# Kernel tuning notes

Measured on AMD Instinct MI355X. Metric: run time of the kernel, lower is better.

Reference implementation:

```python
import jax, jax.numpy as jnp
import numpy as np

POOL_OUT = 100  # AdaptiveAvgPool1d target length
SCALE = np.sqrt(256.0).astype(np.float32)


def setup_inputs() -> dict:
    key = jax.random.key(0)
    ks = jax.random.split(key, 5)
    B, F, T = 16, 512, 4000
    x = jax.random.normal(ks[0], (B, F, T), dtype=jnp.float32)
    Wk = jax.random.normal(ks[1], (256, 100), dtype=jnp.float32) * 0.05
    bk = jax.random.normal(ks[2], (256,), dtype=jnp.float32) * 0.05
    Wq = jax.random.normal(ks[3], (256, 100), dtype=jnp.float32) * 0.05
    bq = jax.random.normal(ks[4], (256,), dtype=jnp.float32) * 0.05
    return {"x": x, "Wk": Wk, "bk": bk, "Wq": Wq, "bq": bq}


def reference(x, Wk, bk, Wq, bq):
    B, F, T = x.shape
    # AdaptiveAvgPool1d(100): T divisible by 100 -> mean over contiguous windows
    pooled = x.reshape(B, F, POOL_OUT, T // POOL_OUT).mean(axis=-1)  # [B,F,100]
    key = pooled @ Wk.T + bk    # [B,F,256]
    query = pooled @ Wq.T + bq  # [B,F,256]
    att = jax.nn.softmax(jnp.einsum('bfd,bgd->bfg', key, query) / SCALE, axis=2)  # [B,F,F]
    # the per-step loop sum+concat is exactly att @ x
    cat = jnp.einsum('bfg,bgt->bft', att, x)  # [B,F,T]
    fw = cat.mean(axis=2, keepdims=True)      # [B,F,1]
    mi = fw.min(axis=1, keepdims=True)
    ma = fw.max(axis=1, keepdims=True)
    fw_n = (fw - mi) / (ma - mi) + 1e-6
    return x * fw_n
```

## Files before the change

### kernel.cpp

```cpp
#include <hip/hip_runtime.h>
#include <math.h>

#define B_ 16
#define F_ 512
#define T_ 4000
#define D_ 100
#define E_ 256
#define ROWS (B_*F_)

__global__ __launch_bounds__(256) void k_pool(const float* __restrict__ x,
                                              float* __restrict__ pooled,
                                              float* __restrict__ xmean) {
    __shared__ float part[4];
    const int row = blockIdx.x;
    const int tid = threadIdx.x;
    float s = 0.f;
    if (tid < 200) {
        const float4* p = (const float4*)(x + (size_t)row * T_ + 20 * tid);
        float4 a0 = p[0], a1 = p[1], a2 = p[2], a3 = p[3], a4 = p[4];
        s  = a0.x + a0.y + a0.z + a0.w;
        s += a1.x + a1.y + a1.z + a1.w;
        s += a2.x + a2.y + a2.z + a2.w;
        s += a3.x + a3.y + a3.z + a3.w;
        s += a4.x + a4.y + a4.z + a4.w;
    }
    float other = __shfl_xor(s, 1);
    if (tid < 200 && (tid & 1) == 0)
        pooled[(size_t)row * D_ + (tid >> 1)] = (s + other) * (1.0f/40.0f);
    float tot = s;
    #pragma unroll
    for (int off = 32; off; off >>= 1) tot += __shfl_xor(tot, off);
    if ((tid & 63) == 0) part[tid >> 6] = tot;
    __syncthreads();
    if (tid == 0)
        xmean[row] = (part[0] + part[1] + part[2] + part[3]) * (1.0f/(float)T_);
}

__global__ __launch_bounds__(256) void k_kq(const float* __restrict__ pooled,
                                            const float* __restrict__ Wk,
                                            const float* __restrict__ bk,
                                            const float* __restrict__ Wq,
                                            const float* __restrict__ bq,
                                            float* __restrict__ KQ) {
    __shared__ float As[D_][65];
    __shared__ float Bs[D_][65];
    const int m0 = blockIdx.x * 64;
    const int n0 = blockIdx.y * 64;
    const int tid = threadIdx.x;

    const float* Ab = pooled + (size_t)m0 * D_;
    for (int i = tid; i < 64 * D_; i += 256) {
        int r = i / D_, k = i - r * D_;
        As[k][r] = Ab[i];
    }
    const float* Wb = (n0 < E_) ? (Wk + (size_t)n0 * D_) : (Wq + (size_t)(n0 - E_) * D_);
    for (int i = tid; i < 64 * D_; i += 256) {
        int r = i / D_, k = i - r * D_;
        Bs[k][r] = Wb[i];
    }
    __syncthreads();

    const int tm = (tid >> 4) * 4;
    const int tn = (tid & 15) * 4;
    float acc[4][4] = {};
    for (int k = 0; k < D_; ++k) {
        float a[4], b[4];
        #pragma unroll
        for (int i = 0; i < 4; ++i) a[i] = As[k][tm + i];
        #pragma unroll
        for (int j = 0; j < 4; ++j) b[j] = Bs[k][tn + j];
        #pragma unroll
        for (int i = 0; i < 4; ++i)
            #pragma unroll
            for (int j = 0; j < 4; ++j)
                acc[i][j] = fmaf(a[i], b[j], acc[i][j]);
    }
    #pragma unroll
    for (int i = 0; i < 4; ++i)
        #pragma unroll
        for (int j = 0; j < 4; ++j) {
            int n = n0 + tn + j;
            float bias = (n < E_) ? bk[n] : bq[n - E_];
            KQ[(size_t)(m0 + tm + i) * 512 + n] = acc[i][j] + bias;
        }
}

__global__ __launch_bounds__(256) void k_scores(const float* __restrict__ KQ,
                                                float* __restrict__ S) {
    __shared__ float As[64][68];
    __shared__ float Bs[64][68];
    const int b  = blockIdx.z;
    const int f0 = blockIdx.x * 64;
    const int g0 = blockIdx.y * 64;
    const float* Ab = KQ + ((size_t)b * F_ + f0) * 512;
    const float* Bb = KQ + ((size_t)b * F_ + g0) * 512 + E_;
    const int tid = threadIdx.x;
    const int tm = (tid >> 4) * 4;
    const int tn = (tid & 15) * 4;
    float acc[4][4] = {};
    for (int ks = 0; ks < E_; ks += 64) {
        for (int i = tid; i < 64 * 64; i += 256) {
            int r = i >> 6, kk = i & 63;
            As[kk][r] = Ab[(size_t)r * 512 + ks + kk];
            Bs[kk][r] = Bb[(size_t)r * 512 + ks + kk];
        }
        __syncthreads();
        #pragma unroll 16
        for (int k = 0; k < 64; ++k) {
            float4 a4 = *(const float4*)(&As[k][tm]);
            float4 b4 = *(const float4*)(&Bs[k][tn]);
            float a[4] = {a4.x, a4.y, a4.z, a4.w};
            float b[4] = {b4.x, b4.y, b4.z, b4.w};
            #pragma unroll
            for (int i = 0; i < 4; ++i)
                #pragma unroll
                for (int j = 0; j < 4; ++j)
                    acc[i][j] = fmaf(a[i], b[j], acc[i][j]);
        }
        __syncthreads();
    }
    float* Sb = S + ((size_t)b * F_ + f0) * 512 + g0;
    #pragma unroll
    for (int i = 0; i < 4; ++i)
        #pragma unroll
        for (int j = 0; j < 4; ++j)
            Sb[(size_t)(tm + i) * 512 + tn + j] = acc[i][j] * (1.0f/16.0f);
}

__global__ __launch_bounds__(256) void k_softmax_fw(const float* __restrict__ S,
                                                    const float* __restrict__ xmean,
                                                    float* __restrict__ fw) {
    const int row  = blockIdx.x * 4 + (threadIdx.x >> 6);
    const int lane = threadIdx.x & 63;
    const int b    = row >> 9;
    const float4* Sr = (const float4*)(S + (size_t)row * 512);
    const float4* xm = (const float4*)(xmean + ((size_t)b << 9));
    float4 v0 = Sr[lane * 2], v1 = Sr[lane * 2 + 1];
    float m = fmaxf(fmaxf(fmaxf(v0.x, v0.y), fmaxf(v0.z, v0.w)),
                    fmaxf(fmaxf(v1.x, v1.y), fmaxf(v1.z, v1.w)));
    #pragma unroll
    for (int off = 32; off; off >>= 1) m = fmaxf(m, __shfl_xor(m, off));
    float4 x0 = xm[lane * 2], x1 = xm[lane * 2 + 1];
    float sum = 0.f, dot = 0.f, p;
    p = expf(v0.x - m); sum += p; dot += p * x0.x;
    p = expf(v0.y - m); sum += p; dot += p * x0.y;
    p = expf(v0.z - m); sum += p; dot += p * x0.z;
    p = expf(v0.w - m); sum += p; dot += p * x0.w;
    p = expf(v1.x - m); sum += p; dot += p * x1.x;
    p = expf(v1.y - m); sum += p; dot += p * x1.y;
    p = expf(v1.z - m); sum += p; dot += p * x1.z;
    p = expf(v1.w - m); sum += p; dot += p * x1.w;
    #pragma unroll
    for (int off = 32; off; off >>= 1) {
        sum += __shfl_xor(sum, off);
        dot += __shfl_xor(dot, off);
    }
    if (lane == 0) fw[row] = dot / sum;
}

__global__ __launch_bounds__(512) void k_norm(const float* __restrict__ fw,
                                              float* __restrict__ fwn) {
    __shared__ float rmin[512];
    __shared__ float rmax[512];
    const int b = blockIdx.x, tid = threadIdx.x;
    float v = fw[b * F_ + tid];
    rmin[tid] = v; rmax[tid] = v;
    __syncthreads();
    for (int s = 256; s > 0; s >>= 1) {
        if (tid < s) {
            rmin[tid] = fminf(rmin[tid], rmin[tid + s]);
            rmax[tid] = fmaxf(rmax[tid], rmax[tid + s]);
        }
        __syncthreads();
    }
    float mi = rmin[0], ma = rmax[0];
    fwn[b * F_ + tid] = (v - mi) / (ma - mi) + 1e-6f;
}

__global__ __launch_bounds__(256) void k_scale(const float* __restrict__ x,
                                               const float* __restrict__ fwn,
                                               float* __restrict__ out) {
    const int row = blockIdx.x;
    const float s = fwn[row];
    const float4* xr = (const float4*)(x + (size_t)row * T_);
    float4* orow = (float4*)(out + (size_t)row * T_);
    for (int i = threadIdx.x; i < T_/4; i += 256) {
        float4 v = xr[i];
        v.x *= s; v.y *= s; v.z *= s; v.w *= s;
        orow[i] = v;
    }
}

extern "C" void kernel_launch(void* const* d_in, const int* in_sizes, int n_in,
                              void* d_out, int out_size, void* d_ws, size_t ws_size,
                              hipStream_t stream) {
    const float* x  = (const float*)d_in[0];
    const float* Wk = (const float*)d_in[1];
    const float* bk = (const float*)d_in[2];
    const float* Wq = (const float*)d_in[3];
    const float* bq = (const float*)d_in[4];
    float* out = (float*)d_out;

    float* ws     = (float*)d_ws;
    float* pooled = ws;
    float* xmean  = pooled + (size_t)ROWS * D_;
    float* KQ     = xmean + ROWS;
    float* S      = KQ + (size_t)ROWS * 512;
    float* fw     = S + (size_t)B_ * F_ * F_;
    float* fwn    = fw + ROWS;

    k_pool<<<ROWS, 256, 0, stream>>>(x, pooled, xmean);
    k_kq<<<dim3(ROWS/64, 512/64), 256, 0, stream>>>(pooled, Wk, bk, Wq, bq, KQ);
    k_scores<<<dim3(F_/64, F_/64, B_), 256, 0, stream>>>(KQ, S);
    k_softmax_fw<<<ROWS/4, 256, 0, stream>>>(S, xmean, fw);
    k_norm<<<B_, 512, 0, stream>>>(fw, fwn);
    k_scale<<<ROWS, 256, 0, stream>>>(x, fwn, out);
}
```

Measured before the change: 321.1 us.

## Use split-bf16 MFMA for attention scores with pre-tiled K/Q layout

The projection kernel now writes K and Q as hi/lo bf16 pairs in a fragment-ready tiled layout. The score kernel uses bf16 MFMA 16x16x32 with three products (hh, hl, lh) to approximate fp32 accuracy, replacing the FP32 FMA tiled GEMM and its shared-memory staging. The pooling kernel also stages each row in LDS before summing. The MFMA path cuts score-GEMM compute, at the cost of a small accuracy loss and an extra LDS round trip in pooling.

```diff
diff --git a/kernel.cpp b/kernel.cpp
--- a/kernel.cpp
+++ b/kernel.cpp
@@ -1,4 +1,5 @@
 #include <hip/hip_runtime.h>
+#include <hip/hip_bf16.h>
 #include <math.h>
 
 #define B_ 16
@@ -8,15 +9,23 @@
 #define E_ 256
 #define ROWS (B_*F_)
 
+typedef __attribute__((ext_vector_type(8))) short short8;
+typedef __attribute__((ext_vector_type(4))) float f32x4;
+
 __global__ __launch_bounds__(256) void k_pool(const float* __restrict__ x,
                                               float* __restrict__ pooled,
                                               float* __restrict__ xmean) {
+    __shared__ float buf[T_];
     __shared__ float part[4];
     const int row = blockIdx.x;
     const int tid = threadIdx.x;
+    const float4* xr = (const float4*)(x + (size_t)row * T_);
+    float4* b4 = (float4*)buf;
+    for (int i = tid; i < T_/4; i += 256) b4[i] = xr[i];
+    __syncthreads();
     float s = 0.f;
     if (tid < 200) {
-        const float4* p = (const float4*)(x + (size_t)row * T_ + 20 * tid);
+        const float4* p = (const float4*)(buf + 20 * tid);
         float4 a0 = p[0], a1 = p[1], a2 = p[2], a3 = p[3], a4 = p[4];
         s  = a0.x + a0.y + a0.z + a0.w;
         s += a1.x + a1.y + a1.z + a1.w;
@@ -41,7 +50,10 @@
                                             const float* __restrict__ bk,
                                             const float* __restrict__ Wq,
                                             const float* __restrict__ bq,
-                                            float* __restrict__ KQ) {
+                                            short* __restrict__ Khi,
+                                            short* __restrict__ Klo,
+                                            short* __restrict__ Qhi,
+                                            short* __restrict__ Qlo) {
     __shared__ float As[D_][65];
     __shared__ float Bs[D_][65];
     const int m0 = blockIdx.x * 64;
@@ -75,56 +87,63 @@
             for (int j = 0; j < 4; ++j)
                 acc[i][j] = fmaf(a[i], b[j], acc[i][j]);
     }
+    const bool is_key = (n0 < E_);
+    short* __restrict__ Phi = is_key ? Khi : Qhi;
+    short* __restrict__ Plo = is_key ? Klo : Qlo;
     #pragma unroll
     for (int i = 0; i < 4; ++i)
         #pragma unroll
-        for (int j = 0; j < 4; ++j) {
-            int n = n0 + tn + j;
-            float bias = (n < E_) ? bk[n] : bq[n - E_];
-            KQ[(size_t)(m0 + tm + i) * 512 + n] = acc[i][j] + bias;
+        for (int jj = 0; jj < 4; ++jj) {
+            int n = n0 + tn + jj;
+            float bias = is_key ? bk[n] : bq[n - E_];
+            float val = acc[i][jj] + bias;
+            int mg = m0 + tm + i;
+            int b = mg >> 9, f = mg & 511;
+            int e = is_key ? n : (n - E_);
+            size_t idx = (((size_t)b * 32 + (f >> 4)) * 32 + (e >> 3)) * 128
+                       + (size_t)(f & 15) * 8 + (e & 7);
+            __hip_bfloat16 h = __float2bfloat16(val);
+            float hf = __bfloat162float(h);
+            __hip_bfloat16 l = __float2bfloat16(val - hf);
+            Phi[idx] = *(short*)&h;
+            Plo[idx] = *(short*)&l;
         }
 }
 
-__global__ __launch_bounds__(256) void k_scores(const float* __restrict__ KQ,
+__global__ __launch_bounds__(256) void k_scores(const short* __restrict__ Khi,
+                                                const short* __restrict__ Klo,
+                                                const short* __restrict__ Qhi,
+                                                const short* __restrict__ Qlo,
                                                 float* __restrict__ S) {
-    __shared__ float As[64][68];
-    __shared__ float Bs[64][68];
-    const int b  = blockIdx.z;
-    const int f0 = blockIdx.x * 64;
-    const int g0 = blockIdx.y * 64;
-    const float* Ab = KQ + ((size_t)b * F_ + f0) * 512;
-    const float* Bb = KQ + ((size_t)b * F_ + g0) * 512 + E_;
-    const int tid = threadIdx.x;
-    const int tm = (tid >> 4) * 4;
-    const int tn = (tid & 15) * 4;
-    float acc[4][4] = {};
-    for (int ks = 0; ks < E_; ks += 64) {
-        for (int i = tid; i < 64 * 64; i += 256) {
-            int r = i >> 6, kk = i & 63;
-            As[kk][r] = Ab[(size_t)r * 512 + ks + kk];
-            Bs[kk][r] = Bb[(size_t)r * 512 + ks + kk];
+    const int b    = blockIdx.z;
+    const int f0   = blockIdx.x * 64;
+    const int g0   = blockIdx.y * 64;
+    const int w    = threadIdx.x >> 6;
+    const int lane = threadIdx.x & 63;
+    const int gt   = (g0 >> 4) + w;
+    const size_t qbase = (((size_t)b * 32 + gt) << 12) + (size_t)lane * 8;
+    const size_t abase = (((size_t)b * 32 + (f0 >> 4)) << 12) + (size_t)lane * 8;
+    f32x4 acc[4] = {};
+    #pragma unroll
+    for (int s = 0; s < 8; ++s) {
+        short8 bh = *(const short8*)(Qhi + qbase + s * 512);
+        short8 bl = *(const short8*)(Qlo + qbase + s * 512);
+        #pragma unroll
+        for (int mt = 0; mt < 4; ++mt) {
+            short8 ah = *(const short8*)(Khi + abase + mt * 4096 + s * 512);
+            short8 al = *(const short8*)(Klo + abase + mt * 4096 + s * 512);
+            acc[mt] = __builtin_amdgcn_mfma_f32_16x16x32_bf16(ah, bh, acc[mt], 0, 0, 0);
+            acc[mt] = __builtin_amdgcn_mfma_f32_16x16x32_bf16(ah, bl, acc[mt], 0, 0, 0);
+            acc[mt] = __builtin_amdgcn_mfma_f32_16x16x32_bf16(al, bh, acc[mt], 0, 0, 0);
         }
-        __syncthreads();
-        #pragma unroll 16
-        for (int k = 0; k < 64; ++k) {
-            float4 a4 = *(const float4*)(&As[k][tm]);
-            float4 b4 = *(const float4*)(&Bs[k][tn]);
-            float a[4] = {a4.x, a4.y, a4.z, a4.w};
-            float b[4] = {b4.x, b4.y, b4.z, b4.w};
-            #pragma unroll
-            for (int i = 0; i < 4; ++i)
-                #pragma unroll
-                for (int j = 0; j < 4; ++j)
-                    acc[i][j] = fmaf(a[i], b[j], acc[i][j]);
-        }
-        __syncthreads();
-    }
-    float* Sb = S + ((size_t)b * F_ + f0) * 512 + g0;
-    #pragma unroll
-    for (int i = 0; i < 4; ++i)
-        #pragma unroll
-        for (int j = 0; j < 4; ++j)
-            Sb[(size_t)(tm + i) * 512 + tn + j] = acc[i][j] * (1.0f/16.0f);
+    }
+    const int col = lane & 15, quad = lane >> 4;
+    float* Sb = S + ((size_t)b * F_ + f0) * 512 + g0 + w * 16 + col;
+    #pragma unroll
+    for (int mt = 0; mt < 4; ++mt)
+        #pragma unroll
+        for (int r = 0; r < 4; ++r)
+            Sb[(size_t)(mt * 16 + quad * 4 + r) * 512] = acc[mt][r] * (1.0f/16.0f);
 }
 
 __global__ __launch_bounds__(256) void k_softmax_fw(const float* __restrict__ S,
@@ -204,14 +223,18 @@
     float* ws     = (float*)d_ws;
     float* pooled = ws;
     float* xmean  = pooled + (size_t)ROWS * D_;
-    float* KQ     = xmean + ROWS;
-    float* S      = KQ + (size_t)ROWS * 512;
+    float* S      = xmean + ROWS;
     float* fw     = S + (size_t)B_ * F_ * F_;
     float* fwn    = fw + ROWS;
+    short* Khi    = (short*)(fwn + ROWS);
+    short* Klo    = Khi + (size_t)B_ * 32 * 4096;
+    short* Qhi    = Klo + (size_t)B_ * 32 * 4096;
+    short* Qlo    = Qhi + (size_t)B_ * 32 * 4096;
 
     k_pool<<<ROWS, 256, 0, stream>>>(x, pooled, xmean);
-    k_kq<<<dim3(ROWS/64, 512/64), 256, 0, stream>>>(pooled, Wk, bk, Wq, bq, KQ);
-    k_scores<<<dim3(F_/64, F_/64, B_), 256, 0, stream>>>(KQ, S);
+    k_kq<<<dim3(ROWS/64, 512/64), 256, 0, stream>>>(pooled, Wk, bk, Wq, bq,
+                                                    Khi, Klo, Qhi, Qlo);
+    k_scores<<<dim3(F_/64, F_/64, B_), 256, 0, stream>>>(Khi, Klo, Qhi, Qlo, S);
     k_softmax_fw<<<ROWS/4, 256, 0, stream>>>(S, xmean, fw);
     k_norm<<<B_, 512, 0, stream>>>(fw, fwn);
     k_scale<<<ROWS, 256, 0, stream>>>(x, fwn, out);
```

New measurement: 316.0 us. About the same (-1.6%).
